# Optimization experiments

Measured on AMD Instinct MI355X. Metric: run time of the kernel, lower is better.

The kernel has to match this reference:

```python
import jax, jax.numpy as jnp
import numpy as np

EMBED = 128          # embed_dim
HID = 128            # hidden_dim (must equal embed_dim for the view math to work)
HEADS = 4
HEAD_DIM = EMBED // HEADS  # = HID // HEADS = 32
N = 50000            # source cells
M = 50000            # target cells
E = 400000           # edges (nnz of inter_neighborhood)


def setup_inputs() -> dict:
    key = jax.random.key(0)
    ks = jax.random.split(key, 13)
    s = lambda d: 1.0 / np.sqrt(d)
    return {
        "source_features": jax.random.normal(ks[0], (N, EMBED), jnp.float32),
        "target_features": jax.random.normal(ks[1], (M, EMBED), jnp.float32),
        "edge_targets": jax.random.randint(ks[2], (E,), 0, M, dtype=jnp.int32),
        "edge_sources": jax.random.randint(ks[3], (E,), 0, N, dtype=jnp.int32),
        "Ws": jax.random.normal(ks[4], (EMBED, HEADS * HID), jnp.float32) * s(EMBED),
        "bs": jnp.zeros((HEADS * HID,), jnp.float32),
        "Wt": jax.random.normal(ks[5], (EMBED, HEADS * HID), jnp.float32) * s(EMBED),
        "bt": jnp.zeros((HEADS * HID,), jnp.float32),
        "attn_w": jax.random.normal(ks[6], (HEADS, HID), jnp.float32),
        "Wm": jax.random.normal(ks[7], (EMBED, EMBED), jnp.float32) * s(EMBED),
        "bm": jnp.zeros((EMBED,), jnp.float32),
        "Wo": jax.random.normal(ks[8], (EMBED, EMBED), jnp.float32) * s(EMBED),
        "bo": jnp.zeros((EMBED,), jnp.float32),
    }


def reference(source_features, target_features, edge_targets, edge_sources,
              Ws, bs, Wt, bt, attn_w, Wm, bm, Wo, bo):
    # Gather endpoint features per edge: [E, EMBED]
    src = source_features[edge_sources]
    tgt = target_features[edge_targets]
    # Fused linear + GELU attention hidden: [E, HEADS, HID]
    hidden = jax.nn.gelu((src @ Ws + bs) + (tgt @ Wt + bt), approximate=False)
    hidden = hidden.reshape(E, HEADS, HID)
    # Attention logits per edge/head: [E, HEADS]
    logits = jnp.einsum('ehd,hd->eh', hidden, attn_w)
    # Scatter-softmax over edges sharing the same target node
    mx = jax.ops.segment_max(logits, edge_targets, num_segments=M)
    ex = jnp.exp(logits - mx[edge_targets])
    den = jax.ops.segment_sum(ex, edge_targets, num_segments=M)
    scores = ex / den[edge_targets]                      # [E, HEADS]
    # Messages: [E, HEADS, HEAD_DIM], weighted and scatter-summed to targets
    msgs = (src @ Wm + bm).reshape(E, HEADS, HEAD_DIM) * scores[..., None]
    agg = jax.ops.segment_sum(msgs, edge_targets, num_segments=M)
    agg = agg.reshape(M, HEADS * HEAD_DIM)               # [M, EMBED]
    return agg @ Wo + bo
```

## Files before the change

kernel.cpp:

```cpp
#include <hip/hip_runtime.h>
#include <math.h>


typedef __bf16 bf16x8 __attribute__((ext_vector_type(8)));
typedef float  f32x4  __attribute__((ext_vector_type(4)));
typedef float  f32x2  __attribute__((ext_vector_type(2)));

__device__ __forceinline__ unsigned short f2bf(float x) {
    unsigned u = __float_as_uint(x);
    u += 0x7FFFu + ((u >> 16) & 1u);
    return (unsigned short)(u >> 16);
}
__device__ __forceinline__ float bf2f(unsigned short b) {
    return __uint_as_float(((unsigned)b) << 16);
}
__device__ __forceinline__ f32x2 up2(unsigned u) {
    f32x2 r;
    r.x = __uint_as_float(u << 16);
    r.y = __uint_as_float(u & 0xFFFF0000u);
    return r;
}
__device__ __forceinline__ float exp2_fast(float x) {
#if __has_builtin(__builtin_amdgcn_exp2f)
    return __builtin_amdgcn_exp2f(x);
#else
    return exp2f(x);
#endif
}

__device__ __forceinline__ f32x2 gelu2(f32x2 v) {
    f32x2 v2 = v * v;
    f32x2 u  = v * (v2 * 0.10294355f + 2.30220820f);
    f32x2 e;
    e.x = exp2_fast(u.x);
    e.y = exp2_fast(u.y);
    f32x2 r;
    r.x = __builtin_amdgcn_rcpf(e.x + 1.0f);
    r.y = __builtin_amdgcn_rcpf(e.y + 1.0f);
    return v - v * r;
}

__device__ __forceinline__ float edge_logit(uint4 h,
    f32x2 ht0, f32x2 ht1, f32x2 ht2, f32x2 ht3,
    f32x2 aw0, f32x2 aw1, f32x2 aw2, f32x2 aw3) {
    f32x2 qv = gelu2(up2(h.x) + ht0) * aw0;
    qv += gelu2(up2(h.y) + ht1) * aw1;
    qv += gelu2(up2(h.z) + ht2) * aw2;
    qv += gelu2(up2(h.w) + ht3) * aw3;
    return qv.x + qv.y;
}

__global__ __launch_bounds__(128)
void prep_weights_kernel(const float* __restrict__ Ws, const float* __restrict__ Wm,
                         const float* __restrict__ Wt, const float* __restrict__ Wo,
                         const float* __restrict__ bs, const float* __restrict__ bm,
                         unsigned short* __restrict__ WThi, unsigned short* __restrict__ WTlo,
                         float* __restrict__ bias_cat) {
    int n = blockIdx.x, k = threadIdx.x;
    float w;
    if      (n < 512)  w = Ws[(size_t)k * 512 + n];
    else if (n < 640)  w = Wm[(size_t)k * 128 + (n - 512)];
    else if (n < 1152) w = Wt[(size_t)k * 512 + (n - 640)];
    else               w = Wo[(size_t)k * 128 + (n - 1152)];
    unsigned short hi = f2bf(w);
    WThi[(size_t)n * 128 + k] = hi;
    WTlo[(size_t)n * 128 + k] = f2bf(w - bf2f(hi));
    if (k == 0 && n < 640) bias_cat[n] = (n < 512) ? bs[n] : bm[n - 512];
}

__global__ void hist_kernel(const int* __restrict__ tgt, int* __restrict__ counts, int E) {
    int e = blockIdx.x * blockDim.x + threadIdx.x;
    if (e < E) atomicAdd(&counts[tgt[e]], 1);
}

__global__ __launch_bounds__(256)
void scan_partial_kernel(const int* __restrict__ counts, int* __restrict__ partials, int M) {
    __shared__ int sdata[256];
    int b = blockIdx.x, tid = threadIdx.x;
    int base = b * 1024 + tid * 4;
    int s = 0;
#pragma unroll
    for (int k = 0; k < 4; ++k) { int idx = base + k; if (idx < M) s += counts[idx]; }
    sdata[tid] = s; __syncthreads();
    for (int d = 128; d > 0; d >>= 1) {
        if (tid < d) sdata[tid] += sdata[tid + d];
        __syncthreads();
    }
    if (tid == 0) partials[b] = sdata[0];
}

__global__ __launch_bounds__(64)
void scan_partials_kernel(const int* __restrict__ partials, int* __restrict__ pbase,
                          int* __restrict__ offsets, int P, int M) {
    int lane = threadIdx.x;
    int own = (lane < P) ? partials[lane] : 0;
    int v = own;
    for (int d = 1; d < 64; d <<= 1) {
        int o = __shfl_up(v, d);
        if (lane >= d) v += o;
    }
    if (lane < P) pbase[lane] = v - own;
    if (lane == 63) offsets[M] = v;
}

__global__ __launch_bounds__(256)
void scan_final_kernel(const int* __restrict__ counts, const int* __restrict__ pbase,
                       int* __restrict__ offsets, int M) {
    __shared__ int sdata[256];
    int b = blockIdx.x, tid = threadIdx.x;
    int base = b * 1024 + tid * 4;
    int c0 = 0, c1 = 0, c2 = 0, c3 = 0;
    if (base + 0 < M) c0 = counts[base + 0];
    if (base + 1 < M) c1 = counts[base + 1];
    if (base + 2 < M) c2 = counts[base + 2];
    if (base + 3 < M) c3 = counts[base + 3];
    int s = c0 + c1 + c2 + c3;
    sdata[tid] = s; __syncthreads();
    int v = s;
    for (int d = 1; d < 256; d <<= 1) {
        int o = (tid >= d) ? sdata[tid - d] : 0;
        __syncthreads();
        v += o;
        sdata[tid] = v;
        __syncthreads();
    }
    int ex = pbase[b] + v - s;
    if (base + 0 < M) offsets[base + 0] = ex;
    if (base + 1 < M) offsets[base + 1] = ex + c0;
    if (base + 2 < M) offsets[base + 2] = ex + c0 + c1;
    if (base + 3 < M) offsets[base + 3] = ex + c0 + c1 + c2;
}

__global__ void scatter_kernel(const int* __restrict__ tgt, const int* __restrict__ src,
                               const int* __restrict__ offsets,
                               int* __restrict__ cursor, int* __restrict__ srcs_sorted, int E) {
    int e = blockIdx.x * blockDim.x + threadIdx.x;
    if (e < E) {
        int t = tgt[e];
        int r = atomicAdd(&cursor[t], 1);
        srcs_sorted[offsets[t] + r] = src[e];
    }
}

__global__ __launch_bounds__(256, 4)
void gemm_hidden_kernel(const float* __restrict__ src_f, const float* __restrict__ tgt_f,
                        const unsigned short* __restrict__ WThi, const unsigned short* __restrict__ WTlo,
                        const float* __restrict__ bias_cat, const float* __restrict__ bt,
                        unsigned short* __restrict__ Hs, unsigned short* __restrict__ Hm,
                        unsigned short* __restrict__ Ht, int N, int M) {
    __shared__ unsigned short Ahi[64 * 72], Alo[64 * 72];
    __shared__ unsigned short Bhi[64 * 72], Blo[64 * 72];

    int i = blockIdx.x;
    int x = i & 7;
    int k = i >> 3;
    int cb = k % 18;
    int rg = k / 18;
    int row_tile = rg * 8 + x;

    bool side1 = cb >= 10;
    const float* Af = side1 ? tgt_f : src_f;
    int rows = side1 ? M : N;
    int row0 = row_tile * 64;
    if (row0 >= rows) return;
    int colL = side1 ? (cb - 10) * 64 : cb * 64;
    int colW = side1 ? 640 + colL : colL;
    const float* bias = side1 ? bt : bias_cat;

    int tid = threadIdx.x;
    int wid = tid >> 6, lane = tid & 63;
    int wm = (wid >> 1) * 32, wn = (wid & 1) * 32;
    int g = lane >> 4, r16 = lane & 15;

    f32x4 acc00 = {0.f, 0.f, 0.f, 0.f}, acc01 = acc00, acc10 = acc00, acc11 = acc00;

    for (int kb = 0; kb < 128; kb += 64) {
#pragma unroll
        for (int l = 0; l < 2; ++l) {
            int idx = l * 256 + tid;
            int r = idx >> 3, c8 = idx & 7;
            int row = row0 + r;
            float4 v0 = make_float4(0.f, 0.f, 0.f, 0.f), v1 = v0;
            if (row < rows) {
                v0 = *(const float4*)(Af + (size_t)row * 128 + kb + c8 * 8);
                v1 = *(const float4*)(Af + (size_t)row * 128 + kb + c8 * 8 + 4);
            }
            ushort4 h0, h1, o0, o1;
            h0.x = f2bf(v0.x); o0.x = f2bf(v0.x - bf2f(h0.x));
            h0.y = f2bf(v0.y); o0.y = f2bf(v0.y - bf2f(h0.y));
            h0.z = f2bf(v0.z); o0.z = f2bf(v0.z - bf2f(h0.z));
            h0.w = f2bf(v0.w); o0.w = f2bf(v0.w - bf2f(h0.w));
            h1.x = f2bf(v1.x); o1.x = f2bf(v1.x - bf2f(h1.x));
            h1.y = f2bf(v1.y); o1.y = f2bf(v1.y - bf2f(h1.y));
            h1.z = f2bf(v1.z); o1.z = f2bf(v1.z - bf2f(h1.z));
            h1.w = f2bf(v1.w); o1.w = f2bf(v1.w - bf2f(h1.w));
            *(ushort4*)(&Ahi[r * 72 + c8 * 8])     = h0;
            *(ushort4*)(&Ahi[r * 72 + c8 * 8 + 4]) = h1;
            *(ushort4*)(&Alo[r * 72 + c8 * 8])     = o0;
            *(ushort4*)(&Alo[r * 72 + c8 * 8 + 4]) = o1;
            uint4 wh = *(const uint4*)(WThi + (size_t)(colW + r) * 128 + kb + c8 * 8);
            uint4 wl = *(const uint4*)(WTlo + (size_t)(colW + r) * 128 + kb + c8 * 8);
            *(uint4*)(&Bhi[r * 72 + c8 * 8]) = wh;
            *(uint4*)(&Blo[r * 72 + c8 * 8]) = wl;
        }
        __syncthreads();

#pragma unroll
        for (int kk = 0; kk < 2; ++kk) {
            int k0 = kk * 32 + g * 8;
            bf16x8 ah0 = *(const bf16x8*)(&Ahi[(wm + r16) * 72 + k0]);
            bf16x8 ah1 = *(const bf16x8*)(&Ahi[(wm + 16 + r16) * 72 + k0]);
            bf16x8 al0 = *(const bf16x8*)(&Alo[(wm + r16) * 72 + k0]);
            bf16x8 al1 = *(const bf16x8*)(&Alo[(wm + 16 + r16) * 72 + k0]);
            bf16x8 bh0 = *(const bf16x8*)(&Bhi[(wn + r16) * 72 + k0]);
            bf16x8 bh1 = *(const bf16x8*)(&Bhi[(wn + 16 + r16) * 72 + k0]);
            bf16x8 bl0 = *(const bf16x8*)(&Blo[(wn + r16) * 72 + k0]);
            bf16x8 bl1 = *(const bf16x8*)(&Blo[(wn + 16 + r16) * 72 + k0]);
            acc00 = __builtin_amdgcn_mfma_f32_16x16x32_bf16(ah0, bh0, acc00, 0, 0, 0);
            acc00 = __builtin_amdgcn_mfma_f32_16x16x32_bf16(ah0, bl0, acc00, 0, 0, 0);
            acc00 = __builtin_amdgcn_mfma_f32_16x16x32_bf16(al0, bh0, acc00, 0, 0, 0);
            acc01 = __builtin_amdgcn_mfma_f32_16x16x32_bf16(ah0, bh1, acc01, 0, 0, 0);
            acc01 = __builtin_amdgcn_mfma_f32_16x16x32_bf16(ah0, bl1, acc01, 0, 0, 0);
            acc01 = __builtin_amdgcn_mfma_f32_16x16x32_bf16(al0, bh1, acc01, 0, 0, 0);
            acc10 = __builtin_amdgcn_mfma_f32_16x16x32_bf16(ah1, bh0, acc10, 0, 0, 0);
            acc10 = __builtin_amdgcn_mfma_f32_16x16x32_bf16(ah1, bl0, acc10, 0, 0, 0);
            acc10 = __builtin_amdgcn_mfma_f32_16x16x32_bf16(al1, bh0, acc10, 0, 0, 0);
            acc11 = __builtin_amdgcn_mfma_f32_16x16x32_bf16(ah1, bh1, acc11, 0, 0, 0);
            acc11 = __builtin_amdgcn_mfma_f32_16x16x32_bf16(ah1, bl1, acc11, 0, 0, 0);
            acc11 = __builtin_amdgcn_mfma_f32_16x16x32_bf16(al1, bh1, acc11, 0, 0, 0);
        }
        __syncthreads();
    }

    int c0 = colL + wn + r16;
    int c1 = c0 + 16;
    float bv0 = bias[c0], bv1 = bias[c1];
#pragma unroll
    for (int ii = 0; ii < 4; ++ii) {
        int rA = row0 + wm + g * 4 + ii;
        int rB = rA + 16;
        if (rA < rows) {
            float o0 = acc00[ii] + bv0, o1 = acc01[ii] + bv1;
            if (side1) {
                Ht[(size_t)rA * 512 + c0] = f2bf(o0);
                Ht[(size_t)rA * 512 + c1] = f2bf(o1);
            } else {
                if (c0 < 512) Hs[(size_t)rA * 512 + c0] = f2bf(o0);
                else          Hm[(size_t)rA * 128 + (c0 - 512)] = f2bf(o0);
                if (c1 < 512) Hs[(size_t)rA * 512 + c1] = f2bf(o1);
                else          Hm[(size_t)rA * 128 + (c1 - 512)] = f2bf(o1);
            }
        }
        if (rB < rows) {
            float o0 = acc10[ii] + bv0, o1 = acc11[ii] + bv1;
            if (side1) {
                Ht[(size_t)rB * 512 + c0] = f2bf(o0);
                Ht[(size_t)rB * 512 + c1] = f2bf(o1);
            } else {
                if (c0 < 512) Hs[(size_t)rB * 512 + c0] = f2bf(o0);
                else          Hm[(size_t)rB * 128 + (c0 - 512)] = f2bf(o0);
                if (c1 < 512) Hs[(size_t)rB * 512 + c1] = f2bf(o1);
                else          Hm[(size_t)rB * 128 + (c1 - 512)] = f2bf(o1);
            }
        }
    }
}

__global__ __launch_bounds__(256, 4)
void gemm_out_kernel(const unsigned short* __restrict__ A,
                     const unsigned short* __restrict__ BT,
                     const float* __restrict__ bias,
                     float* __restrict__ C, int Mrows, int Ntot) {
    __shared__ unsigned short As[64 * 136];
    __shared__ unsigned short Bs[64 * 136];
    int tid = threadIdx.x;
    int row0 = blockIdx.y * 64, col0 = blockIdx.x * 64;

#pragma unroll
    for (int l = 0; l < 4; ++l) {
        int idx = l * 256 + tid;
        int r = idx >> 4, c8 = idx & 15;
        int row = row0 + r;
        uint4 v = make_uint4(0, 0, 0, 0);
        if (row < Mrows) v = *(const uint4*)(A + (size_t)row * 128 + c8 * 8);
        *(uint4*)(&As[r * 136 + c8 * 8]) = v;
    }
#pragma unroll
    for (int l = 0; l < 4; ++l) {
        int idx = l * 256 + tid;
        int r = idx >> 4, c8 = idx & 15;
        uint4 v = *(const uint4*)(BT + (size_t)(col0 + r) * 128 + c8 * 8);
        *(uint4*)(&Bs[r * 136 + c8 * 8]) = v;
    }
    __syncthreads();

    int wid = tid >> 6, lane = tid & 63;
    int wm = (wid >> 1) * 32, wn = (wid & 1) * 32;
    int g = lane >> 4, r16 = lane & 15;

    f32x4 acc00 = {0.f, 0.f, 0.f, 0.f}, acc01 = acc00, acc10 = acc00, acc11 = acc00;

#pragma unroll
    for (int kk = 0; kk < 4; ++kk) {
        int k0 = kk * 32 + g * 8;
        bf16x8 a0 = *(const bf16x8*)(&As[(wm + r16) * 136 + k0]);
        bf16x8 a1 = *(const bf16x8*)(&As[(wm + 16 + r16) * 136 + k0]);
        bf16x8 b0 = *(const bf16x8*)(&Bs[(wn + r16) * 136 + k0]);
        bf16x8 b1 = *(const bf16x8*)(&Bs[(wn + 16 + r16) * 136 + k0]);
        acc00 = __builtin_amdgcn_mfma_f32_16x16x32_bf16(a0, b0, acc00, 0, 0, 0);
        acc01 = __builtin_amdgcn_mfma_f32_16x16x32_bf16(a0, b1, acc01, 0, 0, 0);
        acc10 = __builtin_amdgcn_mfma_f32_16x16x32_bf16(a1, b0, acc10, 0, 0, 0);
        acc11 = __builtin_amdgcn_mfma_f32_16x16x32_bf16(a1, b1, acc11, 0, 0, 0);
    }

    float bv0 = bias[col0 + wn + r16];
    float bv1 = bias[col0 + wn + 16 + r16];
#pragma unroll
    for (int i = 0; i < 4; ++i) {
        int rA = row0 + wm + g * 4 + i;
        int rB = rA + 16;
        if (rA < Mrows) {
            C[(size_t)rA * Ntot + col0 + wn + r16]      = acc00[i] + bv0;
            C[(size_t)rA * Ntot + col0 + wn + 16 + r16] = acc01[i] + bv1;
        }
        if (rB < Mrows) {
            C[(size_t)rB * Ntot + col0 + wn + r16]      = acc10[i] + bv0;
            C[(size_t)rB * Ntot + col0 + wn + 16 + r16] = acc11[i] + bv1;
        }
    }
}

__global__ __launch_bounds__(256)
void attn_kernel(const unsigned short* __restrict__ Hs, const unsigned short* __restrict__ Ht,
                 const unsigned short* __restrict__ Hm, const float* __restrict__ attn_w,
                 const int* __restrict__ offsets, const int* __restrict__ srcs,
                 unsigned short* __restrict__ agg, int M) {
    int wave = threadIdx.x >> 6;
    int lane = threadIdx.x & 63;
    int t = blockIdx.x * 4 + wave;
    if (t >= M) return;

    int j0 = lane << 3;
    uint4 h = *(const uint4*)(Ht + (size_t)t * 512 + j0);
    f32x2 ht0 = up2(h.x), ht1 = up2(h.y), ht2 = up2(h.z), ht3 = up2(h.w);
    const float L2E = 1.4426950408889634f;
    float4 a0 = *(const float4*)(attn_w + j0);
    float4 a1 = *(const float4*)(attn_w + j0 + 4);
    f32x2 aw0 = {a0.x * L2E, a0.y * L2E};
    f32x2 aw1 = {a0.z * L2E, a0.w * L2E};
    f32x2 aw2 = {a1.x * L2E, a1.y * L2E};
    f32x2 aw3 = {a1.z * L2E, a1.w * L2E};

    int off = offsets[t];
    int end = offsets[t + 1];
    int hm_off = lane << 1;

    float m = -INFINITY, den = 0.f;
    f32x2 acc = {0.f, 0.f};

    int i = off;
    uint4 hA, hB, hC, hD;
    unsigned mA, mB, mC, mD;
    bool have = (end - i) >= 4;
    if (have) {
        int s0 = srcs[i], s1 = srcs[i + 1], s2 = srcs[i + 2], s3 = srcs[i + 3];
        hA = *(const uint4*)(Hs + (size_t)s0 * 512 + j0);
        hB = *(const uint4*)(Hs + (size_t)s1 * 512 + j0);
        hC = *(const uint4*)(Hs + (size_t)s2 * 512 + j0);
        hD = *(const uint4*)(Hs + (size_t)s3 * 512 + j0);
        mA = *(const unsigned*)(Hm + (size_t)s0 * 128 + hm_off);
        mB = *(const unsigned*)(Hm + (size_t)s1 * 128 + hm_off);
        mC = *(const unsigned*)(Hm + (size_t)s2 * 128 + hm_off);
        mD = *(const unsigned*)(Hm + (size_t)s3 * 128 + hm_off);
    }
    while (have) {
        int ni = i + 4;
        bool nhave = (end - ni) >= 4;
        uint4 nhA, nhB, nhC, nhD;
        unsigned nmA, nmB, nmC, nmD;
        if (nhave) {
            int s0 = srcs[ni], s1 = srcs[ni + 1], s2 = srcs[ni + 2], s3 = srcs[ni + 3];
            nhA = *(const uint4*)(Hs + (size_t)s0 * 512 + j0);
            nhB = *(const uint4*)(Hs + (size_t)s1 * 512 + j0);
            nhC = *(const uint4*)(Hs + (size_t)s2 * 512 + j0);
            nhD = *(const uint4*)(Hs + (size_t)s3 * 512 + j0);
            nmA = *(const unsigned*)(Hm + (size_t)s0 * 128 + hm_off);
            nmB = *(const unsigned*)(Hm + (size_t)s1 * 128 + hm_off);
            nmC = *(const unsigned*)(Hm + (size_t)s2 * 128 + hm_off);
            nmD = *(const unsigned*)(Hm + (size_t)s3 * 128 + hm_off);
        }

        float q0 = edge_logit(hA, ht0, ht1, ht2, ht3, aw0, aw1, aw2, aw3);
        float q1 = edge_logit(hB, ht0, ht1, ht2, ht3, aw0, aw1, aw2, aw3);
        float q2 = edge_logit(hC, ht0, ht1, ht2, ht3, aw0, aw1, aw2, aw3);
        float q3 = edge_logit(hD, ht0, ht1, ht2, ht3, aw0, aw1, aw2, aw3);
        q0 += __shfl_xor(q0, 1); q1 += __shfl_xor(q1, 1); q2 += __shfl_xor(q2, 1); q3 += __shfl_xor(q3, 1);
        q0 += __shfl_xor(q0, 2); q1 += __shfl_xor(q1, 2); q2 += __shfl_xor(q2, 2); q3 += __shfl_xor(q3, 2);
        q0 += __shfl_xor(q0, 4); q1 += __shfl_xor(q1, 4); q2 += __shfl_xor(q2, 4); q3 += __shfl_xor(q3, 4);
        q0 += __shfl_xor(q0, 8); q1 += __shfl_xor(q1, 8); q2 += __shfl_xor(q2, 8); q3 += __shfl_xor(q3, 8);

        float nm = fmaxf(fmaxf(fmaxf(q0, q1), fmaxf(q2, q3)), m);
        float sc = exp2_fast(m - nm);
        float p0 = exp2_fast(q0 - nm);
        float p1 = exp2_fast(q1 - nm);
        float p2 = exp2_fast(q2 - nm);
        float p3 = exp2_fast(q3 - nm);
        den = fmaf(den, sc, (p0 + p1) + (p2 + p3));
        acc = acc * sc;
        acc += p0 * up2(mA);
        acc += p1 * up2(mB);
        acc += p2 * up2(mC);
        acc += p3 * up2(mD);
        m = nm;

        i = ni;
        if (nhave) {
            hA = nhA; hB = nhB; hC = nhC; hD = nhD;
            mA = nmA; mB = nmB; mC = nmC; mD = nmD;
        }
        have = nhave;
    }
    for (; i < end; ++i) {
        int s0 = srcs[i];
        uint4 hX = *(const uint4*)(Hs + (size_t)s0 * 512 + j0);
        unsigned mX = *(const unsigned*)(Hm + (size_t)s0 * 128 + hm_off);
        float q0 = edge_logit(hX, ht0, ht1, ht2, ht3, aw0, aw1, aw2, aw3);
        q0 += __shfl_xor(q0, 1);
        q0 += __shfl_xor(q0, 2);
        q0 += __shfl_xor(q0, 4);
        q0 += __shfl_xor(q0, 8);
        float nm = fmaxf(m, q0);
        float sc = exp2_fast(m - nm);
        float p0 = exp2_fast(q0 - nm);
        den = fmaf(den, sc, p0);
        acc = acc * sc + p0 * up2(mX);
        m = nm;
    }
    float r = (end > off) ? __builtin_amdgcn_rcpf(den) : 0.0f;
    ushort2 o;
    o.x = f2bf(acc.x * r);
    o.y = f2bf(acc.y * r);
    *(ushort2*)(agg + (size_t)t * 128 + hm_off) = o;
}

extern "C" void kernel_launch(void* const* d_in, const int* in_sizes, int n_in,
                              void* d_out, int out_size, void* d_ws, size_t ws_size,
                              hipStream_t stream) {
    const float* src_f  = (const float*)d_in[0];
    const float* tgt_f  = (const float*)d_in[1];
    const int*   e_tgt  = (const int*)d_in[2];
    const int*   e_src  = (const int*)d_in[3];
    const float* Ws     = (const float*)d_in[4];
    const float* bs     = (const float*)d_in[5];
    const float* Wt     = (const float*)d_in[6];
    const float* bt     = (const float*)d_in[7];
    const float* attn_w = (const float*)d_in[8];
    const float* Wm     = (const float*)d_in[9];
    const float* bm     = (const float*)d_in[10];
    const float* Wo     = (const float*)d_in[11];
    const float* bo     = (const float*)d_in[12];

    int N = in_sizes[0] / 128;
    int M = in_sizes[1] / 128;
    int E = in_sizes[2];

    char* ws = (char*)d_ws;
    size_t woff = 0;
    auto alloc = [&](size_t bytes) -> void* {
        void* p = ws + woff;
        woff += ((bytes + 255) / 256) * 256;
        return p;
    };
    unsigned short* Hs       = (unsigned short*)alloc((size_t)N * 512 * 2);
    unsigned short* Ht       = (unsigned short*)alloc((size_t)M * 512 * 2);
    unsigned short* Hm       = (unsigned short*)alloc((size_t)N * 128 * 2);
    unsigned short* agg_bf   = (unsigned short*)alloc((size_t)M * 128 * 2);
    unsigned short* WThi     = (unsigned short*)alloc((size_t)1280 * 128 * 2);
    unsigned short* WTlo     = (unsigned short*)alloc((size_t)1280 * 128 * 2);
    float*          bias_cat = (float*)alloc(640 * 4);
    int*            counts   = (int*)alloc((size_t)2 * M * 4);
    int*            cursor   = counts + M;
    int*            offsets  = (int*)alloc((size_t)(M + 1) * 4);
    int*            srcs     = (int*)alloc((size_t)E * 4);
    int*            partials = (int*)alloc(64 * 4);
    int*            pbase    = (int*)alloc(64 * 4);

    hipMemsetAsync(counts, 0, (size_t)2 * M * 4, stream);

    const int tb = 256;
    int P = (M + 1023) / 1024;

    hist_kernel<<<(E + tb - 1) / tb, tb, 0, stream>>>(e_tgt, counts, E);
    scan_partial_kernel<<<P, 256, 0, stream>>>(counts, partials, M);
    scan_partials_kernel<<<1, 64, 0, stream>>>(partials, pbase, offsets, P, M);
    scan_final_kernel<<<P, 256, 0, stream>>>(counts, pbase, offsets, M);
    scatter_kernel<<<(E + tb - 1) / tb, tb, 0, stream>>>(e_tgt, e_src, offsets, cursor, srcs, E);

    prep_weights_kernel<<<1280, 128, 0, stream>>>(Ws, Wm, Wt, Wo, bs, bm, WThi, WTlo, bias_cat);

    int rowsMax = (N > M) ? N : M;
    int nRowTiles = (rowsMax + 63) / 64;
    int nRG = (nRowTiles + 7) / 8;
    gemm_hidden_kernel<<<8 * 18 * nRG, 256, 0, stream>>>(src_f, tgt_f, WThi, WTlo,
                                                         bias_cat, bt, Hs, Hm, Ht, N, M);

    attn_kernel<<<(M + 3) / 4, 256, 0, stream>>>(Hs, Ht, Hm, attn_w, offsets, srcs, agg_bf, M);

    dim3 go(128 / 64, (M + 63) / 64);
    gemm_out_kernel<<<go, 256, 0, stream>>>(agg_bf, WThi + (size_t)1152 * 128, bo,
                                            (float*)d_out, M, 128);
}
```

Before: 362.6 us.

## Keep full-K A row tile resident and loop over all output column blocks

The hidden-projection GEMM now gives each block one 64-row tile across all column blocks (10 for source, 8 for target). The full K=128 hi/lo bf16 split of the input is loaded and converted into LDS once and held in registers. Weight fragments are read directly from global/L2 instead of being staged through shared memory. The input split now truncates instead of rounding, and the output conversion uses a simpler rounding. This removes the redundant re-reading and re-conversion of input rows per column block, at the cost of fewer blocks, more registers and uncached-in-LDS weight loads.

```diff
diff --git a/kernel.cpp b/kernel.cpp
--- a/kernel.cpp
+++ b/kernel.cpp
@@ -13,6 +13,15 @@
 }
 __device__ __forceinline__ float bf2f(unsigned short b) {
     return __uint_as_float(((unsigned)b) << 16);
+}
+__device__ __forceinline__ unsigned pack_tr(float a, float b) {
+    return (__float_as_uint(a) >> 16) | (__float_as_uint(b) & 0xFFFF0000u);
+}
+__device__ __forceinline__ float res16(float x) {
+    return x - __uint_as_float(__float_as_uint(x) & 0xFFFF0000u);
+}
+__device__ __forceinline__ unsigned short bf_rn(float x) {
+    return (unsigned short)((__float_as_uint(x) + 0x8000u) >> 16);
 }
 __device__ __forceinline__ f32x2 up2(unsigned u) {
     f32x2 r;
@@ -147,120 +156,102 @@
                         const unsigned short* __restrict__ WThi, const unsigned short* __restrict__ WTlo,
                         const float* __restrict__ bias_cat, const float* __restrict__ bt,
                         unsigned short* __restrict__ Hs, unsigned short* __restrict__ Hm,
-                        unsigned short* __restrict__ Ht, int N, int M) {
-    __shared__ unsigned short Ahi[64 * 72], Alo[64 * 72];
-    __shared__ unsigned short Bhi[64 * 72], Blo[64 * 72];
-
-    int i = blockIdx.x;
-    int x = i & 7;
-    int k = i >> 3;
-    int cb = k % 18;
-    int rg = k / 18;
-    int row_tile = rg * 8 + x;
-
-    bool side1 = cb >= 10;
+                        unsigned short* __restrict__ Ht, int N, int M, int nT0) {
+    __shared__ unsigned short Ahi[64 * 136];
+    __shared__ unsigned short Alo[64 * 136];
+
+    int bx = blockIdx.x;
+    bool side1 = bx >= nT0;
     const float* Af = side1 ? tgt_f : src_f;
     int rows = side1 ? M : N;
-    int row0 = row_tile * 64;
-    if (row0 >= rows) return;
-    int colL = side1 ? (cb - 10) * 64 : cb * 64;
-    int colW = side1 ? 640 + colL : colL;
+    int row0 = (side1 ? bx - nT0 : bx) * 64;
+    int nCols = side1 ? 8 : 10;
+    int colWbase = side1 ? 640 : 0;
     const float* bias = side1 ? bt : bias_cat;
 
     int tid = threadIdx.x;
+
+#pragma unroll
+    for (int l = 0; l < 4; ++l) {
+        int idx = l * 256 + tid;
+        int r = idx >> 4, c8 = idx & 15;
+        int row = row0 + r;
+        float4 v0 = make_float4(0.f, 0.f, 0.f, 0.f), v1 = v0;
+        if (row < rows) {
+            v0 = *(const float4*)(Af + (size_t)row * 128 + c8 * 8);
+            v1 = *(const float4*)(Af + (size_t)row * 128 + c8 * 8 + 4);
+        }
+        uint4 hp, lp;
+        hp.x = pack_tr(v0.x, v0.y); hp.y = pack_tr(v0.z, v0.w);
+        hp.z = pack_tr(v1.x, v1.y); hp.w = pack_tr(v1.z, v1.w);
+        lp.x = pack_tr(res16(v0.x), res16(v0.y)); lp.y = pack_tr(res16(v0.z), res16(v0.w));
+        lp.z = pack_tr(res16(v1.x), res16(v1.y)); lp.w = pack_tr(res16(v1.z), res16(v1.w));
+        *(uint4*)(&Ahi[r * 136 + c8 * 8]) = hp;
+        *(uint4*)(&Alo[r * 136 + c8 * 8]) = lp;
+    }
+    __syncthreads();
+
     int wid = tid >> 6, lane = tid & 63;
     int wm = (wid >> 1) * 32, wn = (wid & 1) * 32;
     int g = lane >> 4, r16 = lane & 15;
 
-    f32x4 acc00 = {0.f, 0.f, 0.f, 0.f}, acc01 = acc00, acc10 = acc00, acc11 = acc00;
-
-    for (int kb = 0; kb < 128; kb += 64) {
-#pragma unroll
-        for (int l = 0; l < 2; ++l) {
-            int idx = l * 256 + tid;
-            int r = idx >> 3, c8 = idx & 7;
-            int row = row0 + r;
-            float4 v0 = make_float4(0.f, 0.f, 0.f, 0.f), v1 = v0;
-            if (row < rows) {
-                v0 = *(const float4*)(Af + (size_t)row * 128 + kb + c8 * 8);
-                v1 = *(const float4*)(Af + (size_t)row * 128 + kb + c8 * 8 + 4);
+    bf16x8 Ah0[4], Ah1[4], Al0[4], Al1[4];
+#pragma unroll
+    for (int kk = 0; kk < 4; ++kk) {
+        int k0 = kk * 32 + g * 8;
+        Ah0[kk] = *(const bf16x8*)(&Ahi[(wm + r16) * 136 + k0]);
+        Ah1[kk] = *(const bf16x8*)(&Ahi[(wm + 16 + r16) * 136 + k0]);
+        Al0[kk] = *(const bf16x8*)(&Alo[(wm + r16) * 136 + k0]);
+        Al1[kk] = *(const bf16x8*)(&Alo[(wm + 16 + r16) * 136 + k0]);
+    }
+
+    for (int c = 0; c < nCols; ++c) {
+        int colW = colWbase + c * 64;
+        const unsigned short* Bh0p = WThi + (size_t)(colW + wn + r16) * 128;
+        const unsigned short* Bh1p = Bh0p + 16 * 128;
+        const unsigned short* Bl0p = WTlo + (size_t)(colW + wn + r16) * 128;
+        const unsigned short* Bl1p = Bl0p + 16 * 128;
+
+        f32x4 acc00 = {0.f, 0.f, 0.f, 0.f}, acc01 = acc00, acc10 = acc00, acc11 = acc00;
+#pragma unroll
+        for (int kk = 0; kk < 4; ++kk) {
+            int k0 = kk * 32 + g * 8;
+            bf16x8 bh0 = *(const bf16x8*)(Bh0p + k0);
+            bf16x8 bh1 = *(const bf16x8*)(Bh1p + k0);
+            bf16x8 bl0 = *(const bf16x8*)(Bl0p + k0);
+            bf16x8 bl1 = *(const bf16x8*)(Bl1p + k0);
+            acc00 = __builtin_amdgcn_mfma_f32_16x16x32_bf16(Ah0[kk], bh0, acc00, 0, 0, 0);
+            acc00 = __builtin_amdgcn_mfma_f32_16x16x32_bf16(Ah0[kk], bl0, acc00, 0, 0, 0);
+            acc00 = __builtin_amdgcn_mfma_f32_16x16x32_bf16(Al0[kk], bh0, acc00, 0, 0, 0);
+            acc01 = __builtin_amdgcn_mfma_f32_16x16x32_bf16(Ah0[kk], bh1, acc01, 0, 0, 0);
+            acc01 = __builtin_amdgcn_mfma_f32_16x16x32_bf16(Ah0[kk], bl1, acc01, 0, 0, 0);
+            acc01 = __builtin_amdgcn_mfma_f32_16x16x32_bf16(Al0[kk], bh1, acc01, 0, 0, 0);
+            acc10 = __builtin_amdgcn_mfma_f32_16x16x32_bf16(Ah1[kk], bh0, acc10, 0, 0, 0);
+            acc10 = __builtin_amdgcn_mfma_f32_16x16x32_bf16(Ah1[kk], bl0, acc10, 0, 0, 0);
+            acc10 = __builtin_amdgcn_mfma_f32_16x16x32_bf16(Al1[kk], bh0, acc10, 0, 0, 0);
+            acc11 = __builtin_amdgcn_mfma_f32_16x16x32_bf16(Ah1[kk], bh1, acc11, 0, 0, 0);
+            acc11 = __builtin_amdgcn_mfma_f32_16x16x32_bf16(Ah1[kk], bl1, acc11, 0, 0, 0);
+            acc11 = __builtin_amdgcn_mfma_f32_16x16x32_bf16(Al1[kk], bh1, acc11, 0, 0, 0);
+        }
+
+        int c0 = c * 64 + wn + r16;
+        int c1 = c0 + 16;
+        float bv0 = bias[c0], bv1 = bias[c1];
+        unsigned short* out; int stride, oc0, oc1;
+        if (side1)        { out = Ht; stride = 512; oc0 = c0;       oc1 = c1; }
+        else if (c0 < 512){ out = Hs; stride = 512; oc0 = c0;       oc1 = c1; }
+        else              { out = Hm; stride = 128; oc0 = c0 - 512; oc1 = c1 - 512; }
+#pragma unroll
+        for (int ii = 0; ii < 4; ++ii) {
+            int rA = row0 + wm + g * 4 + ii;
+            int rB = rA + 16;
+            if (rA < rows) {
+                out[(size_t)rA * stride + oc0] = bf_rn(acc00[ii] + bv0);
+                out[(size_t)rA * stride + oc1] = bf_rn(acc01[ii] + bv1);
             }
-            ushort4 h0, h1, o0, o1;
-            h0.x = f2bf(v0.x); o0.x = f2bf(v0.x - bf2f(h0.x));
-            h0.y = f2bf(v0.y); o0.y = f2bf(v0.y - bf2f(h0.y));
-            h0.z = f2bf(v0.z); o0.z = f2bf(v0.z - bf2f(h0.z));
-            h0.w = f2bf(v0.w); o0.w = f2bf(v0.w - bf2f(h0.w));
-            h1.x = f2bf(v1.x); o1.x = f2bf(v1.x - bf2f(h1.x));
-            h1.y = f2bf(v1.y); o1.y = f2bf(v1.y - bf2f(h1.y));
-            h1.z = f2bf(v1.z); o1.z = f2bf(v1.z - bf2f(h1.z));
-            h1.w = f2bf(v1.w); o1.w = f2bf(v1.w - bf2f(h1.w));
-            *(ushort4*)(&Ahi[r * 72 + c8 * 8])     = h0;
-            *(ushort4*)(&Ahi[r * 72 + c8 * 8 + 4]) = h1;
-            *(ushort4*)(&Alo[r * 72 + c8 * 8])     = o0;
-            *(ushort4*)(&Alo[r * 72 + c8 * 8 + 4]) = o1;
-            uint4 wh = *(const uint4*)(WThi + (size_t)(colW + r) * 128 + kb + c8 * 8);
-            uint4 wl = *(const uint4*)(WTlo + (size_t)(colW + r) * 128 + kb + c8 * 8);
-            *(uint4*)(&Bhi[r * 72 + c8 * 8]) = wh;
-            *(uint4*)(&Blo[r * 72 + c8 * 8]) = wl;
-        }
-        __syncthreads();
-
-#pragma unroll
-        for (int kk = 0; kk < 2; ++kk) {
-            int k0 = kk * 32 + g * 8;
-            bf16x8 ah0 = *(const bf16x8*)(&Ahi[(wm + r16) * 72 + k0]);
-            bf16x8 ah1 = *(const bf16x8*)(&Ahi[(wm + 16 + r16) * 72 + k0]);
-            bf16x8 al0 = *(const bf16x8*)(&Alo[(wm + r16) * 72 + k0]);
-            bf16x8 al1 = *(const bf16x8*)(&Alo[(wm + 16 + r16) * 72 + k0]);
-            bf16x8 bh0 = *(const bf16x8*)(&Bhi[(wn + r16) * 72 + k0]);
-            bf16x8 bh1 = *(const bf16x8*)(&Bhi[(wn + 16 + r16) * 72 + k0]);
-            bf16x8 bl0 = *(const bf16x8*)(&Blo[(wn + r16) * 72 + k0]);
-            bf16x8 bl1 = *(const bf16x8*)(&Blo[(wn + 16 + r16) * 72 + k0]);
-            acc00 = __builtin_amdgcn_mfma_f32_16x16x32_bf16(ah0, bh0, acc00, 0, 0, 0);
-            acc00 = __builtin_amdgcn_mfma_f32_16x16x32_bf16(ah0, bl0, acc00, 0, 0, 0);
-            acc00 = __builtin_amdgcn_mfma_f32_16x16x32_bf16(al0, bh0, acc00, 0, 0, 0);
-            acc01 = __builtin_amdgcn_mfma_f32_16x16x32_bf16(ah0, bh1, acc01, 0, 0, 0);
-            acc01 = __builtin_amdgcn_mfma_f32_16x16x32_bf16(ah0, bl1, acc01, 0, 0, 0);
-            acc01 = __builtin_amdgcn_mfma_f32_16x16x32_bf16(al0, bh1, acc01, 0, 0, 0);
-            acc10 = __builtin_amdgcn_mfma_f32_16x16x32_bf16(ah1, bh0, acc10, 0, 0, 0);
-            acc10 = __builtin_amdgcn_mfma_f32_16x16x32_bf16(ah1, bl0, acc10, 0, 0, 0);
-            acc10 = __builtin_amdgcn_mfma_f32_16x16x32_bf16(al1, bh0, acc10, 0, 0, 0);
-            acc11 = __builtin_amdgcn_mfma_f32_16x16x32_bf16(ah1, bh1, acc11, 0, 0, 0);
-            acc11 = __builtin_amdgcn_mfma_f32_16x16x32_bf16(ah1, bl1, acc11, 0, 0, 0);
-            acc11 = __builtin_amdgcn_mfma_f32_16x16x32_bf16(al1, bh1, acc11, 0, 0, 0);
-        }
-        __syncthreads();
-    }
-
-    int c0 = colL + wn + r16;
-    int c1 = c0 + 16;
-    float bv0 = bias[c0], bv1 = bias[c1];
-#pragma unroll
-    for (int ii = 0; ii < 4; ++ii) {
-        int rA = row0 + wm + g * 4 + ii;
-        int rB = rA + 16;
-        if (rA < rows) {
-            float o0 = acc00[ii] + bv0, o1 = acc01[ii] + bv1;
-            if (side1) {
-                Ht[(size_t)rA * 512 + c0] = f2bf(o0);
-                Ht[(size_t)rA * 512 + c1] = f2bf(o1);
-            } else {
-                if (c0 < 512) Hs[(size_t)rA * 512 + c0] = f2bf(o0);
-                else          Hm[(size_t)rA * 128 + (c0 - 512)] = f2bf(o0);
-                if (c1 < 512) Hs[(size_t)rA * 512 + c1] = f2bf(o1);
-                else          Hm[(size_t)rA * 128 + (c1 - 512)] = f2bf(o1);
-            }
-        }
-        if (rB < rows) {
-            float o0 = acc10[ii] + bv0, o1 = acc11[ii] + bv1;
-            if (side1) {
-                Ht[(size_t)rB * 512 + c0] = f2bf(o0);
-                Ht[(size_t)rB * 512 + c1] = f2bf(o1);
-            } else {
-                if (c0 < 512) Hs[(size_t)rB * 512 + c0] = f2bf(o0);
-                else          Hm[(size_t)rB * 128 + (c0 - 512)] = f2bf(o0);
-                if (c1 < 512) Hs[(size_t)rB * 512 + c1] = f2bf(o1);
-                else          Hm[(size_t)rB * 128 + (c1 - 512)] = f2bf(o1);
+            if (rB < rows) {
+                out[(size_t)rB * stride + oc0] = bf_rn(acc10[ii] + bv0);
+                out[(size_t)rB * stride + oc1] = bf_rn(acc11[ii] + bv1);
             }
         }
     }
@@ -498,11 +489,9 @@
 
     prep_weights_kernel<<<1280, 128, 0, stream>>>(Ws, Wm, Wt, Wo, bs, bm, WThi, WTlo, bias_cat);
 
-    int rowsMax = (N > M) ? N : M;
-    int nRowTiles = (rowsMax + 63) / 64;
-    int nRG = (nRowTiles + 7) / 8;
-    gemm_hidden_kernel<<<8 * 18 * nRG, 256, 0, stream>>>(src_f, tgt_f, WThi, WTlo,
-                                                         bias_cat, bt, Hs, Hm, Ht, N, M);
+    int nT0 = (N + 63) / 64, nT1 = (M + 63) / 64;
+    gemm_hidden_kernel<<<nT0 + nT1, 256, 0, stream>>>(src_f, tgt_f, WThi, WTlo,
+                                                      bias_cat, bt, Hs, Hm, Ht, N, M, nT0);
 
     attn_kernel<<<(M + 3) / 4, 256, 0, stream>>>(Hs, Ht, Hm, attn_w, offsets, srcs, agg_bf, M);
 
```

Measured after the change: 408.1 us. +12.5%, slower.
